# Kernel tuning notes

Measured on AMD Instinct MI355X. Metric: run time of the kernel, lower is better.

## Reference

```python
import jax, jax.numpy as jnp
from jax import lax
import numpy as np

NUM_NODES = 32
C = 64
EPS = 1e-5

# Static random DAG: edge i->j (i<j) with prob 0.25; node index == topological order.
_rng = np.random.default_rng(0)
_adj = _rng.random((NUM_NODES, NUM_NODES)) < 0.25
PRED = [tuple(i for i in range(j) if _adj[i, j]) for j in range(NUM_NODES)]
SUCC = [tuple(j for j in range(i + 1, NUM_NODES) if _adj[i, j]) for i in range(NUM_NODES)]
ISPAN = [max(s) if s else NUM_NODES for s in SUCC]
# Nodes whose outputs survive the torch live/delete bookkeeping at the final stack:
# sinks (ispan == NUM_NODES) plus predecessors of the last topological node.
FINAL = [i for i in range(NUM_NODES) if ISPAN[i] >= NUM_NODES - 1]


def _sep_conv(y, dw, pw, stride):
    # depthwise 3x3 (torch padding=1) then pointwise 1x1
    y = lax.conv_general_dilated(y, dw, (stride, stride), ((1, 1), (1, 1)),
                                 feature_group_count=C,
                                 dimension_numbers=('NCHW', 'OIHW', 'NCHW'))
    return jnp.einsum('oc,nchw->nohw', pw, y)


def _bn(y, g, b, m, v):
    inv = (g / jnp.sqrt(v + EPS))[None, :, None, None]
    return (y - m[None, :, None, None]) * inv + b[None, :, None, None]


def _forward(x, dw, pw, gamma, beta, mean, var, agg_w):
    outs = [None] * NUM_NODES
    for i in range(NUM_NODES):  # static structural loop over the fixed DAG
        preds = PRED[i]
        if len(preds) == 0:          # input node: consumes x, downsample stride 2
            y, stride = x, 2
        elif len(preds) == 1:        # single predecessor: plain pass-through (squeeze)
            y, stride = outs[preds[0]], 1
        else:                         # sigmoid-weighted sum of predecessor outputs
            w = jax.nn.sigmoid(agg_w[i, :len(preds)])
            y = jnp.einsum('pnchw,p->nchw', jnp.stack([outs[p] for p in preds]), w)
            stride = 1
        h = _sep_conv(jax.nn.relu(y), dw[i], pw[i], stride)
        outs[i] = _bn(h, gamma[i], beta[i], mean[i], var[i])
    return jnp.mean(jnp.stack([outs[i] for i in FINAL]), axis=0)


def setup_inputs():
    key = jax.random.key(0)
    ks = jax.random.split(key, 8)
    B, H, W = 8, 112, 112
    x = jax.random.normal(ks[0], (B, C, H, W), jnp.float32)
    # fan-in scaling keeps activations bounded across the up-to-32-deep DAG
    dw = jax.random.normal(ks[1], (NUM_NODES, C, 1, 3, 3), jnp.float32) / 3.0
    pw = jax.random.normal(ks[2], (NUM_NODES, C, C), jnp.float32) / 8.0
    gamma = jax.random.uniform(ks[3], (NUM_NODES, C), jnp.float32, 0.5, 1.5)
    beta = jax.random.normal(ks[4], (NUM_NODES, C), jnp.float32) * 0.1
    mean = jax.random.normal(ks[5], (NUM_NODES, C), jnp.float32) * 0.1
    var = jax.random.uniform(ks[6], (NUM_NODES, C), jnp.float32, 0.5, 1.5)
    agg_w = jax.random.normal(ks[7], (NUM_NODES, NUM_NODES), jnp.float32)
    return {"x": x, "dw": dw, "pw": pw, "gamma": gamma, "beta": beta,
            "mean": mean, "var": var, "agg_w": agg_w}


def reference(x, dw, pw, gamma, beta, mean, var, agg_w):
    return _forward(x, dw, pw, gamma, beta, mean, var, agg_w)
```

## Files before the change

kernel.cpp:

```cpp
#include <hip/hip_runtime.h>
#include <cstdint>
#include <cstddef>

#define NN 32
#define NODE_ELEMS 1605632

typedef unsigned __int128 u128;
typedef __attribute__((ext_vector_type(8))) short bf16x8;
typedef __attribute__((ext_vector_type(4))) float f32x4;

static void compute_adj(bool adj[NN][NN]) {
  uint32_t pool[4];
  uint32_t hc = 0x43b0d7e5u;
  auto hashmix = [&hc](uint32_t v) -> uint32_t {
    v ^= hc; hc *= 0x931e8875u; v *= hc; v ^= v >> 16; return v;
  };
  auto mix = [](uint32_t x, uint32_t y) -> uint32_t {
    uint32_t r = x * 0xca01f9ddu - y * 0x4973f715u; r ^= r >> 16; return r;
  };
  for (int i = 0; i < 4; i++) pool[i] = hashmix(0u);
  for (int s = 0; s < 4; s++)
    for (int d = 0; d < 4; d++)
      if (s != d) pool[d] = mix(pool[d], hashmix(pool[s]));
  uint32_t hb = 0x8b51f9ddu;
  uint32_t w[8];
  for (int k = 0; k < 8; k++) {
    uint32_t v = pool[k & 3];
    v ^= hb; hb *= 0x58f38dedu; v *= hb; v ^= v >> 16;
    w[k] = v;
  }
  uint64_t s64[4];
  for (int j = 0; j < 4; j++) s64[j] = (uint64_t)w[2 * j] | ((uint64_t)w[2 * j + 1] << 32);
  u128 initstate = ((u128)s64[0] << 64) | s64[1];
  u128 initseq   = ((u128)s64[2] << 64) | s64[3];
  const u128 MULT = ((u128)0x2360ED051FC65DA4ULL << 64) | 0x4385DF649FCCF645ULL;
  u128 state = 0;
  u128 inc = (initseq << 1) | 1;
  state = state * MULT + inc;
  state += initstate;
  state = state * MULT + inc;
  for (int i = 0; i < NN; i++)
    for (int j = 0; j < NN; j++) {
      state = state * MULT + inc;
      uint64_t hi = (uint64_t)(state >> 64), lo = (uint64_t)state;
      unsigned rot = (unsigned)(hi >> 58);
      uint64_t xr = hi ^ lo;
      uint64_t out = (xr >> rot) | (xr << ((64u - rot) & 63u));
      double dv = (double)(out >> 11) * (1.0 / 9007199254740992.0);
      adj[i][j] = (dv < 0.25);
    }
}

struct NodeDesc {
  uint8_t node, npred, slot, flags;
  uint8_t pred_slot[31];
  uint8_t pad;
};
struct GroupArg { int n; NodeDesc d[32]; };
struct FinalArg { int nf; uint8_t slot[32]; };

__device__ __forceinline__ float bf2f_lo(unsigned int w) {
  union { unsigned int u; float f; } c; c.u = w << 16; return c.f;
}
__device__ __forceinline__ float bf2f_hi(unsigned int w) {
  union { unsigned int u; float f; } c; c.u = w & 0xFFFF0000u; return c.f;
}
__device__ __forceinline__ float bf2f(unsigned short h) {
  union { unsigned int u; float f; } c; c.u = ((unsigned int)h) << 16; return c.f;
}
__device__ __forceinline__ unsigned short f2bf(float f) {
  union { float f; unsigned int u; } c; c.f = f;
  unsigned int u = c.u + 0x7FFFu + ((c.u >> 16) & 1u);
  return (unsigned short)(u >> 16);
}

__global__ __launch_bounds__(256) void input_kernel(
    GroupArg g,
    const float* __restrict__ x,
    const float* __restrict__ dwall,
    const float* __restrict__ pwall,
    const float* __restrict__ gmall,
    const float* __restrict__ btall,
    const float* __restrict__ mnall,
    const float* __restrict__ vrall,
    unsigned short* __restrict__ wsb)
{
  __shared__ float xtile[9 * 17 * 64];
  __shared__ __align__(16) unsigned short pwb[4096];
  __shared__ __align__(16) unsigned short tbuf[2048];

  const int b = blockIdx.x & 7;
  const int m = blockIdx.x >> 3;
  const int t = threadIdx.x;
  const int ty = (m / 7) * 4;
  const int tx = (m % 7) * 8;

  const int dwc = t & 63;
  const int pbase = (t >> 6) * 8;

  {
    const int r0 = t >> 6;
    const float* xb = x + (size_t)(b * 64 + dwc) * 12544;
    const int iy0 = ty * 2 - 1, ix0 = tx * 2 - 1;
    for (int iyL = r0; iyL < 9; iyL += 4) {
      int gy = iy0 + iyL;
      bool rowok = ((unsigned)gy < 112u);
      const float* row = xb + gy * 112;
      float* dst = xtile + (iyL * 17) * 64 + dwc;
      #pragma unroll
      for (int ixL = 0; ixL < 17; ixL++) {
        int gx = ix0 + ixL;
        float v = 0.f;
        if (rowok && ((unsigned)gx < 112u)) v = fmaxf(row[gx], 0.f);
        dst[ixL * 64] = v;
      }
    }
  }

  for (int kk = 0; kk < g.n; kk++) {
    const NodeDesc nd = g.d[kk];
    const int node = nd.node;

    __syncthreads();

    {
      const float* pwn = pwall + node * 4096;
      #pragma unroll
      for (int i = 0; i < 16; i++) {
        int gidx = t + 256 * i;
        int o = gidx >> 6, cc = gidx & 63;
        pwb[o * 64 + ((((cc >> 3) ^ (o & 7)) << 3) | (cc & 7))] = f2bf(pwn[gidx]);
      }
    }

    const float* k9 = dwall + (node * 64 + dwc) * 9;
    float kk9[9];
    #pragma unroll
    for (int q = 0; q < 9; q++) kk9[q] = k9[q];

    float tv[8];
    #pragma unroll
    for (int jj = 0; jj < 8; jj++) {
      int p = pbase + jj;
      int py = p >> 3, px = p & 7;
      const float* r0 = xtile + ((py * 2) * 17 + px * 2) * 64 + dwc;
      tv[jj] = r0[0]    * kk9[0] + r0[64]   * kk9[1] + r0[128]  * kk9[2]
             + r0[1088] * kk9[3] + r0[1152] * kk9[4] + r0[1216] * kk9[5]
             + r0[2176] * kk9[6] + r0[2240] * kk9[7] + r0[2304] * kk9[8];
    }

    #pragma unroll
    for (int jj = 0; jj < 8; jj++) {
      int p = pbase + jj;
      tbuf[p * 64 + ((((dwc >> 3) ^ (p & 7)) << 3) | (dwc & 7))] = f2bf(tv[jj]);
    }
    __syncthreads();

    const int lane = t & 63;
    const int wave = t >> 6;
    const int mtile = wave & 1;
    const int npair = wave >> 1;
    const int lm = lane & 15;
    const int quad = lane >> 4;

    bf16x8 afrag[2];
    #pragma unroll
    for (int ks = 0; ks < 2; ks++) {
      int pos = mtile * 16 + lm;
      int gg = ks * 4 + quad;
      afrag[ks] = *(const bf16x8*)&tbuf[pos * 64 + ((gg ^ (pos & 7)) << 3)];
    }
    f32x4 acc[2];
    #pragma unroll
    for (int nt = 0; nt < 2; nt++) {
      acc[nt] = (f32x4){0.f, 0.f, 0.f, 0.f};
      int oc = (npair * 2 + nt) * 16 + lm;
      #pragma unroll
      for (int ks = 0; ks < 2; ks++) {
        int gg = ks * 4 + quad;
        bf16x8 bfrag = *(const bf16x8*)&pwb[oc * 64 + ((gg ^ (oc & 7)) << 3)];
        acc[nt] = __builtin_amdgcn_mfma_f32_16x16x32_bf16(afrag[ks], bfrag, acc[nt], 0, 0, 0);
      }
    }

    unsigned short* slotp = wsb + (size_t)nd.slot * NODE_ELEMS;
    #pragma unroll
    for (int nt = 0; nt < 2; nt++) {
      int oc = (npair * 2 + nt) * 16 + lm;
      int gi = node * 64 + oc;
      float inv = gmall[gi] / sqrtf(vrall[gi] + 1e-5f);
      float mn = mnall[gi], btv = btall[gi];
      #pragma unroll
      for (int rr = 0; rr < 4; rr++) {
        int pos = mtile * 16 + quad * 4 + rr;
        int gy = ty + (pos >> 3), gx = tx + (pos & 7);
        size_t base = (((size_t)(b * 56 + gy)) * 56 + gx) * 64 + oc;
        slotp[base] = f2bf((acc[nt][rr] - mn) * inv + btv);
      }
    }
  }
}

__global__ __launch_bounds__(256) void level_kernel(
    GroupArg g,
    const float* __restrict__ dwall,
    const float* __restrict__ pwall,
    const float* __restrict__ gmall,
    const float* __restrict__ btall,
    const float* __restrict__ mnall,
    const float* __restrict__ vrall,
    const float* __restrict__ aggw,
    unsigned short* __restrict__ wsb)
{
  __shared__ float smem[3840];
  __shared__ __align__(16) unsigned short pwb[4096];
  __shared__ __align__(16) unsigned short tbuf[2048];
  __shared__ float wlds[32];

  const int bid = blockIdx.x;
  const int nid = bid / 784;
  const int r   = bid - nid * 784;
  const int b = r & 7;
  const int m = r >> 3;
  const int t = threadIdx.x;
  const int ty = (m / 7) * 4;
  const int tx = (m % 7) * 8;

  const NodeDesc nd = g.d[nid];
  const int node = nd.node;

  const int dwc = t & 63;
  const int pbase = (t >> 6) * 8;

  const float* k9 = dwall + (node * 64 + dwc) * 9;
  float kk9[9];
  #pragma unroll
  for (int q = 0; q < 9; q++) kk9[q] = k9[q];

  float tv[8];

  if (t < nd.npred) {
    float wv = 1.f / (1.f + expf(-aggw[node * 32 + t]));
    wlds[t] = (nd.npred == 1) ? 1.0f : wv;
  }
  const int np = nd.npred;
  float sa[2][8];
  int off[2];
  bool inb[2];
  #pragma unroll
  for (int u = 0; u < 2; u++) {
    int idx = t + u * 256;
    bool valid = (u == 0) || (t < 224);
    int pos = idx >> 3, q8 = idx & 7;
    int hy = pos / 10, hx = pos - hy * 10;
    int gy = ty + hy - 1, gx = tx + hx - 1;
    inb[u] = valid && ((unsigned)gy < 56u) && ((unsigned)gx < 56u);
    off[u] = ((b * 56 + gy) * 56 + gx) * 64 + q8 * 8;
    #pragma unroll
    for (int q = 0; q < 8; q++) sa[u][q] = 0.f;
  }
  __syncthreads();
  for (int p0 = 0; p0 < np; p0 += 4) {
    uint4 v[4][2];
    #pragma unroll
    for (int pp = 0; pp < 4; pp++) {
      if (p0 + pp < np) {
        const unsigned short* pb = wsb + (size_t)nd.pred_slot[p0 + pp] * NODE_ELEMS;
        #pragma unroll
        for (int u = 0; u < 2; u++)
          if (inb[u]) v[pp][u] = *(const uint4*)(pb + off[u]);
      }
    }
    #pragma unroll
    for (int pp = 0; pp < 4; pp++) {
      if (p0 + pp < np) {
        float wv = wlds[p0 + pp];
        #pragma unroll
        for (int u = 0; u < 2; u++) {
          if (inb[u]) {
            sa[u][0] = fmaf(wv, bf2f_lo(v[pp][u].x), sa[u][0]);
            sa[u][1] = fmaf(wv, bf2f_hi(v[pp][u].x), sa[u][1]);
            sa[u][2] = fmaf(wv, bf2f_lo(v[pp][u].y), sa[u][2]);
            sa[u][3] = fmaf(wv, bf2f_hi(v[pp][u].y), sa[u][3]);
            sa[u][4] = fmaf(wv, bf2f_lo(v[pp][u].z), sa[u][4]);
            sa[u][5] = fmaf(wv, bf2f_hi(v[pp][u].z), sa[u][5]);
            sa[u][6] = fmaf(wv, bf2f_lo(v[pp][u].w), sa[u][6]);
            sa[u][7] = fmaf(wv, bf2f_hi(v[pp][u].w), sa[u][7]);
          }
        }
      }
    }
  }
  #pragma unroll
  for (int u = 0; u < 2; u++) {
    int idx = t + u * 256;
    if ((u == 0) || (t < 224)) {
      float4 s0 = make_float4(fmaxf(sa[u][0], 0.f), fmaxf(sa[u][1], 0.f),
                              fmaxf(sa[u][2], 0.f), fmaxf(sa[u][3], 0.f));
      float4 s1 = make_float4(fmaxf(sa[u][4], 0.f), fmaxf(sa[u][5], 0.f),
                              fmaxf(sa[u][6], 0.f), fmaxf(sa[u][7], 0.f));
      *(float4*)&smem[idx * 8] = s0;
      *(float4*)&smem[idx * 8 + 4] = s1;
    }
  }
  {
    const float* pwn = pwall + node * 4096;
    #pragma unroll
    for (int i = 0; i < 16; i++) {
      int gidx = t + 256 * i;
      int o = gidx >> 6, cc = gidx & 63;
      pwb[o * 64 + ((((cc >> 3) ^ (o & 7)) << 3) | (cc & 7))] = f2bf(pwn[gidx]);
    }
  }
  __syncthreads();
  #pragma unroll
  for (int jj = 0; jj < 8; jj++) {
    int p = pbase + jj;
    int py = p >> 3, px = p & 7;
    const float* r0 = smem + (py * 10 + px) * 64 + dwc;
    tv[jj] = r0[0]    * kk9[0] + r0[64]   * kk9[1] + r0[128]  * kk9[2]
           + r0[640]  * kk9[3] + r0[704]  * kk9[4] + r0[768]  * kk9[5]
           + r0[1280] * kk9[6] + r0[1344] * kk9[7] + r0[1408] * kk9[8];
  }

  #pragma unroll
  for (int jj = 0; jj < 8; jj++) {
    int p = pbase + jj;
    tbuf[p * 64 + ((((dwc >> 3) ^ (p & 7)) << 3) | (dwc & 7))] = f2bf(tv[jj]);
  }
  __syncthreads();

  const int lane = t & 63;
  const int wave = t >> 6;
  const int mtile = wave & 1;
  const int npair = wave >> 1;
  const int lm = lane & 15;
  const int quad = lane >> 4;

  bf16x8 afrag[2];
  #pragma unroll
  for (int ks = 0; ks < 2; ks++) {
    int pos = mtile * 16 + lm;
    int gg = ks * 4 + quad;
    afrag[ks] = *(const bf16x8*)&tbuf[pos * 64 + ((gg ^ (pos & 7)) << 3)];
  }
  f32x4 acc[2];
  #pragma unroll
  for (int nt = 0; nt < 2; nt++) {
    acc[nt] = (f32x4){0.f, 0.f, 0.f, 0.f};
    int oc = (npair * 2 + nt) * 16 + lm;
    #pragma unroll
    for (int ks = 0; ks < 2; ks++) {
      int gg = ks * 4 + quad;
      bf16x8 bfrag = *(const bf16x8*)&pwb[oc * 64 + ((gg ^ (oc & 7)) << 3)];
      acc[nt] = __builtin_amdgcn_mfma_f32_16x16x32_bf16(afrag[ks], bfrag, acc[nt], 0, 0, 0);
    }
  }

  unsigned short* slotp = wsb + (size_t)nd.slot * NODE_ELEMS;
  #pragma unroll
  for (int nt = 0; nt < 2; nt++) {
    int oc = (npair * 2 + nt) * 16 + lm;
    int gi = node * 64 + oc;
    float inv = gmall[gi] / sqrtf(vrall[gi] + 1e-5f);
    float mn = mnall[gi], btv = btall[gi];
    #pragma unroll
    for (int rr = 0; rr < 4; rr++) {
      int pos = mtile * 16 + quad * 4 + rr;
      int gy = ty + (pos >> 3), gx = tx + (pos & 7);
      size_t base = (((size_t)(b * 56 + gy)) * 56 + gx) * 64 + oc;
      slotp[base] = f2bf((acc[nt][rr] - mn) * inv + btv);
    }
  }
}

__global__ __launch_bounds__(256) void finalize_kernel(
    FinalArg fa, const unsigned short* __restrict__ wsb,
    float* __restrict__ out, float inv_nf)
{
  __shared__ float lds[64 * 29];
  const int bid = blockIdx.x;
  const int half = bid & 1;
  const int by = bid >> 1;
  const int b = by / 56, y = by - b * 56;
  const int x0 = half * 28;
  const size_t rbase = ((((size_t)b * 56 + y) * 56) + x0) * 64;
  const int t = threadIdx.x;
  const int nf = fa.nf;

  if (t < 224) {
    const int xx = t >> 3, q8 = t & 7;
    const unsigned short* p0 = wsb + rbase + xx * 64 + q8 * 8;
    float s0 = 0.f, s1 = 0.f, s2 = 0.f, s3 = 0.f,
          s4 = 0.f, s5 = 0.f, s6 = 0.f, s7 = 0.f;
    for (int f0 = 0; f0 < nf; f0 += 4) {
      uint4 va, vb, vc, vd;
      if (f0 + 0 < nf) va = *(const uint4*)(p0 + (size_t)fa.slot[f0 + 0] * NODE_ELEMS);
      if (f0 + 1 < nf) vb = *(const uint4*)(p0 + (size_t)fa.slot[f0 + 1] * NODE_ELEMS);
      if (f0 + 2 < nf) vc = *(const uint4*)(p0 + (size_t)fa.slot[f0 + 2] * NODE_ELEMS);
      if (f0 + 3 < nf) vd = *(const uint4*)(p0 + (size_t)fa.slot[f0 + 3] * NODE_ELEMS);
      if (f0 + 0 < nf) {
        s0 += bf2f_lo(va.x); s1 += bf2f_hi(va.x); s2 += bf2f_lo(va.y); s3 += bf2f_hi(va.y);
        s4 += bf2f_lo(va.z); s5 += bf2f_hi(va.z); s6 += bf2f_lo(va.w); s7 += bf2f_hi(va.w);
      }
      if (f0 + 1 < nf) {
        s0 += bf2f_lo(vb.x); s1 += bf2f_hi(vb.x); s2 += bf2f_lo(vb.y); s3 += bf2f_hi(vb.y);
        s4 += bf2f_lo(vb.z); s5 += bf2f_hi(vb.z); s6 += bf2f_lo(vb.w); s7 += bf2f_hi(vb.w);
      }
      if (f0 + 2 < nf) {
        s0 += bf2f_lo(vc.x); s1 += bf2f_hi(vc.x); s2 += bf2f_lo(vc.y); s3 += bf2f_hi(vc.y);
        s4 += bf2f_lo(vc.z); s5 += bf2f_hi(vc.z); s6 += bf2f_lo(vc.w); s7 += bf2f_hi(vc.w);
      }
      if (f0 + 3 < nf) {
        s0 += bf2f_lo(vd.x); s1 += bf2f_hi(vd.x); s2 += bf2f_lo(vd.y); s3 += bf2f_hi(vd.y);
        s4 += bf2f_lo(vd.z); s5 += bf2f_hi(vd.z); s6 += bf2f_lo(vd.w); s7 += bf2f_hi(vd.w);
      }
    }
    float* dl = lds + (q8 * 8) * 29 + xx;
    dl[0 * 29] = s0 * inv_nf; dl[1 * 29] = s1 * inv_nf;
    dl[2 * 29] = s2 * inv_nf; dl[3 * 29] = s3 * inv_nf;
    dl[4 * 29] = s4 * inv_nf; dl[5 * 29] = s5 * inv_nf;
    dl[6 * 29] = s6 * inv_nf; dl[7 * 29] = s7 * inv_nf;
  }
  __syncthreads();
  float* dst = out + (size_t)b * 64 * 3136 + (size_t)y * 56 + x0;
  for (int j = t; j < 1792; j += 256) {
    int c = j / 28, xx = j - c * 28;
    dst[(size_t)c * 3136 + xx] = lds[c * 29 + xx];
  }
}

extern "C" void kernel_launch(void* const* d_in, const int* in_sizes, int n_in,
                              void* d_out, int out_size, void* d_ws, size_t ws_size,
                              hipStream_t stream) {
  (void)in_sizes; (void)n_in; (void)ws_size; (void)out_size;
  const float* x     = (const float*)d_in[0];
  const float* dw    = (const float*)d_in[1];
  const float* pw    = (const float*)d_in[2];
  const float* gamma = (const float*)d_in[3];
  const float* beta  = (const float*)d_in[4];
  const float* mean  = (const float*)d_in[5];
  const float* var   = (const float*)d_in[6];
  const float* aggw  = (const float*)d_in[7];
  unsigned short* wsb = (unsigned short*)d_ws;
  float* out = (float*)d_out;

  bool adj[NN][NN];
  compute_adj(adj);

  int npred[NN], preds[NN][NN], nsucc[NN], ispan[NN], level[NN];
  for (int j = 0; j < NN; j++) {
    npred[j] = 0;
    for (int i = 0; i < j; i++) if (adj[i][j]) preds[j][npred[j]++] = i;
  }
  for (int i = 0; i < NN; i++) {
    nsucc[i] = 0; ispan[i] = NN;
    int mx = -1;
    for (int j = i + 1; j < NN; j++) if (adj[i][j]) { nsucc[i]++; mx = j; }
    if (nsucc[i] > 0) ispan[i] = mx;
  }
  int maxlev = 0;
  for (int j = 0; j < NN; j++) {
    int lv = 0;
    for (int p = 0; p < npred[j]; p++) {
      int cand = level[preds[j][p]] + 1;
      if (cand > lv) lv = cand;
    }
    level[j] = lv;
    if (lv > maxlev) maxlev = lv;
  }
  bool isfinal[NN]; int nf = 0;
  for (int i = 0; i < NN; i++) { isfinal[i] = (ispan[i] >= NN - 1); if (isfinal[i]) nf++; }
  int lastlvl[NN];
  for (int i = 0; i < NN; i++) {
    lastlvl[i] = -1;
    for (int j = i + 1; j < NN; j++) if (adj[i][j] && level[j] > lastlvl[i]) lastlvl[i] = level[j];
  }
  int slot[NN]; bool used[NN];
  for (int s = 0; s < NN; s++) used[s] = false;
  for (int L = 0; L <= maxlev; L++) {
    for (int i = 0; i < NN; i++) {
      if (level[i] != L) continue;
      int s = 0; while (used[s]) s++;
      used[s] = true; slot[i] = s;
    }
    for (int i = 0; i < NN; i++)
      if (level[i] <= L && !isfinal[i] && lastlvl[i] == L)
        used[slot[i]] = false;
  }

  float inv_nf = 1.0f / (float)nf;

  for (int L = 0; L <= maxlev; L++) {
    GroupArg g; g.n = 0;
    for (int i = 0; i < NN; i++) {
      if (level[i] != L) continue;
      NodeDesc& nd = g.d[g.n++];
      nd.node = (uint8_t)i;
      nd.npred = (uint8_t)npred[i];
      nd.slot = (uint8_t)slot[i];
      nd.flags = 0;
      for (int p = 0; p < npred[i]; p++) nd.pred_slot[p] = (uint8_t)slot[preds[i][p]];
    }
    if (g.n > 0) {
      if (L == 0) {
        input_kernel<<<784, 256, 0, stream>>>(g, x, dw, pw, gamma, beta,
                                              mean, var, wsb);
      } else {
        level_kernel<<<784 * g.n, 256, 0, stream>>>(g, dw, pw, gamma, beta,
                                                    mean, var, aggw, wsb);
      }
    }
  }

  FinalArg fa; fa.nf = 0;
  for (int i = 0; i < NN; i++) if (isfinal[i]) fa.slot[fa.nf++] = (uint8_t)slot[i];
  finalize_kernel<<<896, 256, 0, stream>>>(fa, wsb, out, inv_nf);
}
```

Before: 236.7 us.

## Halve level kernel spatial tile, vectorize input loads, compute sigmoid weights in registers

The level kernel tile shrinks from 4x8 to 2x8 output positions, which doubles the block count. Shared memory per block goes down and each wave now issues a single MFMA over 16 output channels. The sigmoid weight precompute in LDS and its barrier are dropped; each thread evaluates the sigmoid itself in registers. The input kernel reads each row with float4 loads in place of scalar loads. The smaller tile raises halo overhead (4 of 10 rows are halo) and reloads the pointwise weights twice as often, in exchange for more parallelism and occupancy.

```diff
diff --git a/kernel.cpp b/kernel.cpp
--- a/kernel.cpp
+++ b/kernel.cpp
@@ -101,19 +101,39 @@
   {
     const int r0 = t >> 6;
     const float* xb = x + (size_t)(b * 64 + dwc) * 12544;
-    const int iy0 = ty * 2 - 1, ix0 = tx * 2 - 1;
+    const int iy0 = ty * 2 - 1;
+    const int xbase = tx * 2 - 4;
     for (int iyL = r0; iyL < 9; iyL += 4) {
       int gy = iy0 + iyL;
       bool rowok = ((unsigned)gy < 112u);
-      const float* row = xb + gy * 112;
+      const float* row = xb + gy * 112 + xbase;
+      float4 z = make_float4(0.f, 0.f, 0.f, 0.f);
+      float4 v0 = z, v1 = z, v2 = z, v3 = z, v4 = z;
+      if (rowok) {
+        if (xbase >= 0) v0 = *(const float4*)(row);
+        v1 = *(const float4*)(row + 4);
+        v2 = *(const float4*)(row + 8);
+        v3 = *(const float4*)(row + 12);
+        v4 = *(const float4*)(row + 16);
+      }
       float* dst = xtile + (iyL * 17) * 64 + dwc;
-      #pragma unroll
-      for (int ixL = 0; ixL < 17; ixL++) {
-        int gx = ix0 + ixL;
-        float v = 0.f;
-        if (rowok && ((unsigned)gx < 112u)) v = fmaxf(row[gx], 0.f);
-        dst[ixL * 64] = v;
-      }
+      dst[0 * 64]  = fmaxf(v0.w, 0.f);
+      dst[1 * 64]  = fmaxf(v1.x, 0.f);
+      dst[2 * 64]  = fmaxf(v1.y, 0.f);
+      dst[3 * 64]  = fmaxf(v1.z, 0.f);
+      dst[4 * 64]  = fmaxf(v1.w, 0.f);
+      dst[5 * 64]  = fmaxf(v2.x, 0.f);
+      dst[6 * 64]  = fmaxf(v2.y, 0.f);
+      dst[7 * 64]  = fmaxf(v2.z, 0.f);
+      dst[8 * 64]  = fmaxf(v2.w, 0.f);
+      dst[9 * 64]  = fmaxf(v3.x, 0.f);
+      dst[10 * 64] = fmaxf(v3.y, 0.f);
+      dst[11 * 64] = fmaxf(v3.z, 0.f);
+      dst[12 * 64] = fmaxf(v3.w, 0.f);
+      dst[13 * 64] = fmaxf(v4.x, 0.f);
+      dst[14 * 64] = fmaxf(v4.y, 0.f);
+      dst[15 * 64] = fmaxf(v4.z, 0.f);
+      dst[16 * 64] = fmaxf(v4.w, 0.f);
     }
   }
 
@@ -212,37 +232,30 @@
     const float* __restrict__ aggw,
     unsigned short* __restrict__ wsb)
 {
-  __shared__ float smem[3840];
+  __shared__ float smem[2560];
   __shared__ __align__(16) unsigned short pwb[4096];
-  __shared__ __align__(16) unsigned short tbuf[2048];
-  __shared__ float wlds[32];
+  __shared__ __align__(16) unsigned short tbuf[1024];
 
   const int bid = blockIdx.x;
-  const int nid = bid / 784;
-  const int r   = bid - nid * 784;
+  const int nid = bid / 1568;
+  const int r   = bid - nid * 1568;
   const int b = r & 7;
   const int m = r >> 3;
   const int t = threadIdx.x;
-  const int ty = (m / 7) * 4;
+  const int ty = (m / 7) * 2;
   const int tx = (m % 7) * 8;
 
   const NodeDesc nd = g.d[nid];
   const int node = nd.node;
 
   const int dwc = t & 63;
-  const int pbase = (t >> 6) * 8;
+  const int pbase = (t >> 6) * 4;
 
   const float* k9 = dwall + (node * 64 + dwc) * 9;
   float kk9[9];
   #pragma unroll
   for (int q = 0; q < 9; q++) kk9[q] = k9[q];
 
-  float tv[8];
-
-  if (t < nd.npred) {
-    float wv = 1.f / (1.f + expf(-aggw[node * 32 + t]));
-    wlds[t] = (nd.npred == 1) ? 1.0f : wv;
-  }
   const int np = nd.npred;
   float sa[2][8];
   int off[2];
@@ -250,7 +263,7 @@
   #pragma unroll
   for (int u = 0; u < 2; u++) {
     int idx = t + u * 256;
-    bool valid = (u == 0) || (t < 224);
+    bool valid = (u == 0) || (t < 64);
     int pos = idx >> 3, q8 = idx & 7;
     int hy = pos / 10, hx = pos - hy * 10;
     int gy = ty + hy - 1, gx = tx + hx - 1;
@@ -259,7 +272,6 @@
     #pragma unroll
     for (int q = 0; q < 8; q++) sa[u][q] = 0.f;
   }
-  __syncthreads();
   for (int p0 = 0; p0 < np; p0 += 4) {
     uint4 v[4][2];
     #pragma unroll
@@ -271,10 +283,16 @@
           if (inb[u]) v[pp][u] = *(const uint4*)(pb + off[u]);
       }
     }
+    float wv4[4];
+    #pragma unroll
+    for (int pp = 0; pp < 4; pp++)
+      if (p0 + pp < np)
+        wv4[pp] = (np == 1) ? 1.0f
+                            : 1.f / (1.f + expf(-aggw[node * 32 + p0 + pp]));
     #pragma unroll
     for (int pp = 0; pp < 4; pp++) {
       if (p0 + pp < np) {
-        float wv = wlds[p0 + pp];
+        float wv = wv4[pp];
         #pragma unroll
         for (int u = 0; u < 2; u++) {
           if (inb[u]) {
@@ -294,7 +312,7 @@
   #pragma unroll
   for (int u = 0; u < 2; u++) {
     int idx = t + u * 256;
-    if ((u == 0) || (t < 224)) {
+    if ((u == 0) || (t < 64)) {
       float4 s0 = make_float4(fmaxf(sa[u][0], 0.f), fmaxf(sa[u][1], 0.f),
                               fmaxf(sa[u][2], 0.f), fmaxf(sa[u][3], 0.f));
       float4 s1 = make_float4(fmaxf(sa[u][4], 0.f), fmaxf(sa[u][5], 0.f),
@@ -313,8 +331,9 @@
     }
   }
   __syncthreads();
-  #pragma unroll
-  for (int jj = 0; jj < 8; jj++) {
+  float tv[4];
+  #pragma unroll
+  for (int jj = 0; jj < 4; jj++) {
     int p = pbase + jj;
     int py = p >> 3, px = p & 7;
     const float* r0 = smem + (py * 10 + px) * 64 + dwc;
@@ -324,7 +343,7 @@
   }
 
   #pragma unroll
-  for (int jj = 0; jj < 8; jj++) {
+  for (int jj = 0; jj < 4; jj++) {
     int p = pbase + jj;
     tbuf[p * 64 + ((((dwc >> 3) ^ (p & 7)) << 3) | (dwc & 7))] = f2bf(tv[jj]);
   }
@@ -332,44 +351,36 @@
 
   const int lane = t & 63;
   const int wave = t >> 6;
-  const int mtile = wave & 1;
-  const int npair = wave >> 1;
   const int lm = lane & 15;
   const int quad = lane >> 4;
 
   bf16x8 afrag[2];
   #pragma unroll
   for (int ks = 0; ks < 2; ks++) {
-    int pos = mtile * 16 + lm;
+    int pos = lm;
     int gg = ks * 4 + quad;
     afrag[ks] = *(const bf16x8*)&tbuf[pos * 64 + ((gg ^ (pos & 7)) << 3)];
   }
-  f32x4 acc[2];
-  #pragma unroll
-  for (int nt = 0; nt < 2; nt++) {
-    acc[nt] = (f32x4){0.f, 0.f, 0.f, 0.f};
-    int oc = (npair * 2 + nt) * 16 + lm;
-    #pragma unroll
-    for (int ks = 0; ks < 2; ks++) {
-      int gg = ks * 4 + quad;
-      bf16x8 bfrag = *(const bf16x8*)&pwb[oc * 64 + ((gg ^ (oc & 7)) << 3)];
-      acc[nt] = __builtin_amdgcn_mfma_f32_16x16x32_bf16(afrag[ks], bfrag, acc[nt], 0, 0, 0);
-    }
+  const int oc = wave * 16 + lm;
+  f32x4 acc = (f32x4){0.f, 0.f, 0.f, 0.f};
+  #pragma unroll
+  for (int ks = 0; ks < 2; ks++) {
+    int gg = ks * 4 + quad;
+    bf16x8 bfrag = *(const bf16x8*)&pwb[oc * 64 + ((gg ^ (oc & 7)) << 3)];
+    acc = __builtin_amdgcn_mfma_f32_16x16x32_bf16(afrag[ks], bfrag, acc, 0, 0, 0);
   }
 
   unsigned short* slotp = wsb + (size_t)nd.slot * NODE_ELEMS;
-  #pragma unroll
-  for (int nt = 0; nt < 2; nt++) {
-    int oc = (npair * 2 + nt) * 16 + lm;
+  {
     int gi = node * 64 + oc;
     float inv = gmall[gi] / sqrtf(vrall[gi] + 1e-5f);
     float mn = mnall[gi], btv = btall[gi];
     #pragma unroll
     for (int rr = 0; rr < 4; rr++) {
-      int pos = mtile * 16 + quad * 4 + rr;
+      int pos = quad * 4 + rr;
       int gy = ty + (pos >> 3), gx = tx + (pos & 7);
       size_t base = (((size_t)(b * 56 + gy)) * 56 + gx) * 64 + oc;
-      slotp[base] = f2bf((acc[nt][rr] - mn) * inv + btv);
+      slotp[base] = f2bf((acc[rr] - mn) * inv + btv);
     }
   }
 }
@@ -507,8 +518,8 @@
         input_kernel<<<784, 256, 0, stream>>>(g, x, dw, pw, gamma, beta,
                                               mean, var, wsb);
       } else {
-        level_kernel<<<784 * g.n, 256, 0, stream>>>(g, dw, pw, gamma, beta,
-                                                    mean, var, aggw, wsb);
+        level_kernel<<<1568 * g.n, 256, 0, stream>>>(g, dw, pw, gamma, beta,
+                                                     mean, var, aggw, wsb);
       }
     }
   }
```

After: 321.1 us. 1.36x slower.
